# Performance work log

Measured on AMD Instinct MI355X. Metric: run time of the kernel, lower is better.

The kernel has to match this reference:

```python
import jax, jax.numpy as jnp
import numpy as np

B, H, W, C, WS, NCLS = 8, 256, 256, 256, 8, 18


def setup_inputs() -> dict:
    key = jax.random.key(0)
    ks = jax.random.split(key, 10)
    s = 1.0 / np.sqrt(C)
    return {
        "x": jax.random.normal(ks[0], (B, H, W, C), jnp.float32),
        "Wq": jax.random.normal(ks[1], (C, NCLS), jnp.float32) * s,
        "bq": jnp.zeros((NCLS,), jnp.float32),
        "Wk": jax.random.normal(ks[2], (C, NCLS), jnp.float32) * s,
        "bk": jnp.zeros((NCLS,), jnp.float32),
        "Wv": jax.random.normal(ks[3], (C, C), jnp.float32) * s,
        "bv": jnp.zeros((C,), jnp.float32),
        "Wres": jax.random.normal(ks[4], (C, C), jnp.float32) * s,
        "bres": jnp.zeros((C,), jnp.float32),
        "gamma": jnp.zeros((1,), jnp.float32) + 0.1,
    }


def _window_partition(x):
    # (B,H,W,C) -> (B*nH*nW, ws*ws, C)
    b, h, w, c = x.shape
    x = x.reshape(b, h // WS, WS, w // WS, WS, c)
    x = jnp.transpose(x, (0, 1, 3, 2, 4, 5))
    return x.reshape(-1, WS * WS, c)


def _window_reverse(xw, c):
    # (B*nH*nW, ws*ws, c) -> (B,H,W,c)
    x = xw.reshape(B, H // WS, W // WS, WS, WS, c)
    x = jnp.transpose(x, (0, 1, 3, 2, 4, 5))
    return x.reshape(B, H, W, c)


def reference(x, Wq, bq, Wk, bk, Wv, bv, Wres, bres, gamma):
    xw = _window_partition(x)                      # (nWin, ws^2, C)
    seg_map = xw @ Wq + bq                         # (nWin, ws^2, n_cls)
    seg_ft = xw @ Wk + bk                          # (nWin, ws^2, n_cls)
    feats = xw @ Wv + bv                           # (nWin, ws^2, C)
    score = jnp.einsum('nik,njk->nij', seg_map, seg_ft)  # (nWin, ws^2, ws^2)
    score = jax.nn.softmax(score, axis=-1)
    feats = jnp.einsum('nij,njc->nic', score, feats)
    feats = feats @ Wres + bres                    # dropout = identity (eval)
    feat_map = gamma * feats + xw
    return _window_reverse(seg_map, NCLS), _window_reverse(feat_map, C)
```

## Files before the change

kernel.cpp:

```cpp
#include <hip/hip_runtime.h>
#include <hip/hip_bf16.h>


typedef __bf16 bf16_t;
typedef __bf16 bf16x8 __attribute__((ext_vector_type(8)));
typedef __bf16 bf16x4 __attribute__((ext_vector_type(4)));
typedef float  f32x4  __attribute__((ext_vector_type(4)));

#define MFMA16(a, b, c) __builtin_amdgcn_mfma_f32_16x16x32_bf16((a), (b), (c), 0, 0, 0)
#define BAR() do { asm volatile("s_waitcnt lgkmcnt(0)" ::: "memory"); \
                   __builtin_amdgcn_s_barrier(); } while (0)

static constexpr int kC = 256, kNCLS = 18;
static constexpr int WQT_OFF = 0;
static constexpr int WKT_OFF = 8192;
static constexpr int WFT_OFF = 16384;
static constexpr int BF_BYTE_OFF = 81920 * 2;

__device__ __forceinline__ int xs_i(int r, int c) { return (r << 8) + (c ^ ((r & 7) << 3)); }
__device__ __forceinline__ int sb_i(int r, int c) { return (r << 6) + (c ^ ((r & 7) << 3)); }

__global__ __launch_bounds__(256) void prep_kernel(
    const float* __restrict__ Wq, const float* __restrict__ Wk,
    const float* __restrict__ Wv, const float* __restrict__ bv,
    const float* __restrict__ Wres, const float* __restrict__ bres,
    bf16_t* __restrict__ wsb, float* __restrict__ bff)
{
  const int blk = blockIdx.x, t = threadIdx.x;
  if (blk < 256) {
    __shared__ float wcol[256];
    const int n = blk;
    wcol[t] = Wres[t * kC + n];
    __syncthreads();
    float acc = 0.f;
    const float* wvrow = Wv + (size_t)t * kC;
#pragma unroll 4
    for (int j = 0; j < 256; j += 4) {
      f32x4 a = *(const f32x4*)(wvrow + j);
      acc += a[0] * wcol[j] + a[1] * wcol[j + 1] + a[2] * wcol[j + 2] + a[3] * wcol[j + 3];
    }
    wsb[WFT_OFF + n * kC + t] = (bf16_t)acc;
  } else if (blk == 256) {
    float acc = bres[t];
    for (int j = 0; j < 256; ++j) acc += bv[j] * Wres[j * kC + t];
    bff[t] = acc;
  } else {
    int tid = (blk - 257) * 256 + t;
    if (tid < 8192) {
      int n = tid >> 8, k = tid & 255;
      wsb[WQT_OFF + tid] = (n < kNCLS) ? (bf16_t)Wq[k * kNCLS + n] : (bf16_t)0.0f;
    } else {
      int u = tid - 8192;
      int n = u >> 8, k = u & 255;
      wsb[WKT_OFF + u] = (n < kNCLS) ? (bf16_t)Wk[k * kNCLS + n] : (bf16_t)0.0f;
    }
  }
}

__global__ __launch_bounds__(256, 2) void semwin_main(
    const float* __restrict__ x,
    const float* __restrict__ bq, const float* __restrict__ bk,
    const float* __restrict__ gamma,
    const bf16_t* __restrict__ wsb, const float* __restrict__ bff,
    float* __restrict__ out0, float* __restrict__ out1)
{
  __shared__ bf16_t xsf0[64 * 256];
  __shared__ bf16_t xsf1[64 * 256];
  __shared__ bf16_t sbf0[64 * 64];
  __shared__ bf16_t sbf1[64 * 64];

  const int tid  = threadIdx.x;
  const int wave = tid >> 6;
  const int lane = tid & 63;
  const int l15  = lane & 15;
  const int g    = lane >> 4;

  const int wid2 = blockIdx.x << 1;
  const int b    = wid2 >> 10;
  const int wh   = (wid2 >> 5) & 31;
  const int ww   = wid2 & 31;
  const int pix0 = (b << 16) + (wh << 11) + (ww << 3);
  const int pix1 = pix0 + 8;

  const f32x4 fzero = {0.f, 0.f, 0.f, 0.f};
  const float gm = gamma[0];

  {
    const int t = tid >> 2;
    const int q = tid & 3;
    const int ro = ((t >> 3) << 8) + (t & 7);
    const float* s0 = x + (size_t)(pix0 + ro) * kC + q * 8;
    const float* s1 = s0 + 8 * kC;
    f32x4 la[8][2], lb[8][2];
#pragma unroll
    for (int i = 0; i < 8; ++i) {
      la[i][0] = *(const f32x4*)(s0 + i * 32);
      la[i][1] = *(const f32x4*)(s0 + i * 32 + 4);
      lb[i][0] = *(const f32x4*)(s1 + i * 32);
      lb[i][1] = *(const f32x4*)(s1 + i * 32 + 4);
    }
#pragma unroll
    for (int i = 0; i < 8; ++i) {
      bf16x8 v0, v1;
#pragma unroll
      for (int r = 0; r < 4; ++r) {
        v0[r] = (bf16_t)la[i][0][r]; v0[4 + r] = (bf16_t)la[i][1][r];
        v1[r] = (bf16_t)lb[i][0][r]; v1[4 + r] = (bf16_t)lb[i][1][r];
      }
      *(bf16x8*)&xsf0[xs_i(t, i * 32 + q * 8)] = v0;
      *(bf16x8*)&xsf1[xs_i(t, i * 32 + q * 8)] = v1;
    }
  }
  BAR();

  {
    const bf16_t* wt   = wsb + ((wave < 2) ? WQT_OFF : WKT_OFF);
    const float*  bias = (wave < 2) ? bq : bk;
    const int mbase = (wave & 1) << 5;
    const int cofs  = (wave < 2) ? 0 : 32;
    const bool isQ  = (wave < 2);
    f32x4 acc[2][2][2];
#pragma unroll
    for (int w2 = 0; w2 < 2; ++w2)
#pragma unroll
      for (int mt = 0; mt < 2; ++mt)
#pragma unroll
        for (int nt = 0; nt < 2; ++nt) acc[w2][mt][nt] = fzero;
#pragma unroll
    for (int k0 = 0; k0 < 256; k0 += 32) {
      bf16x8 b0 = *(const bf16x8*)(wt + l15 * 256 + k0 + g * 8);
      bf16x8 b1 = *(const bf16x8*)(wt + (16 + l15) * 256 + k0 + g * 8);
#pragma unroll
      for (int w2 = 0; w2 < 2; ++w2) {
        const bf16_t* xs = w2 ? xsf1 : xsf0;
        bf16x8 a0 = *(const bf16x8*)&xs[xs_i(mbase + l15, k0 + g * 8)];
        bf16x8 a1 = *(const bf16x8*)&xs[xs_i(mbase + 16 + l15, k0 + g * 8)];
        acc[w2][0][0] = MFMA16(a0, b0, acc[w2][0][0]);
        acc[w2][0][1] = MFMA16(a0, b1, acc[w2][0][1]);
        acc[w2][1][0] = MFMA16(a1, b0, acc[w2][1][0]);
        acc[w2][1][1] = MFMA16(a1, b1, acc[w2][1][1]);
      }
    }
#pragma unroll
    for (int w2 = 0; w2 < 2; ++w2) {
      bf16_t* sb = w2 ? sbf1 : sbf0;
      const int pix = w2 ? pix1 : pix0;
#pragma unroll
      for (int nt = 0; nt < 2; ++nt) {
        const int coln = (nt << 4) + l15;
        const float bval = (coln < kNCLS) ? bias[coln] : 0.f;
#pragma unroll
        for (int mt = 0; mt < 2; ++mt) {
#pragma unroll
          for (int r = 0; r < 4; ++r) {
            const int row = mbase + (mt << 4) + (g << 2) + r;
            const float v = acc[w2][mt][nt][r] + bval;
            sb[sb_i(row, cofs + coln)] = (bf16_t)v;
            if (isQ && coln < kNCLS) {
              out0[(size_t)(pix + ((row >> 3) << 8) + (row & 7)) * kNCLS + coln] = v;
            }
          }
        }
      }
    }
  }
  BAR();

  {
    const int mbase = wave << 4;
    f32x4 s[2][4];
#pragma unroll
    for (int w2 = 0; w2 < 2; ++w2) {
      const bf16_t* sb = w2 ? sbf1 : sbf0;
      const bf16x8 aq = *(const bf16x8*)&sb[sb_i(mbase + l15, g * 8)];
#pragma unroll
      for (int nt = 0; nt < 4; ++nt) {
        bf16x8 bk8 = *(const bf16x8*)&sb[sb_i((nt << 4) + l15, 32 + g * 8)];
        s[w2][nt] = MFMA16(aq, bk8, fzero);
      }
    }
    BAR();
#pragma unroll
    for (int w2 = 0; w2 < 2; ++w2) {
      bf16_t* sb = w2 ? sbf1 : sbf0;
#pragma unroll
      for (int r = 0; r < 4; ++r) {
        float m = fmaxf(fmaxf(s[w2][0][r], s[w2][1][r]), fmaxf(s[w2][2][r], s[w2][3][r]));
#pragma unroll
        for (int off = 1; off < 16; off <<= 1) m = fmaxf(m, __shfl_xor(m, off));
        float e0 = __expf(s[w2][0][r] - m), e1 = __expf(s[w2][1][r] - m);
        float e2 = __expf(s[w2][2][r] - m), e3 = __expf(s[w2][3][r] - m);
        float sum = (e0 + e1) + (e2 + e3);
#pragma unroll
        for (int off = 1; off < 16; off <<= 1) sum += __shfl_xor(sum, off);
        const float inv = 1.0f / sum;
        const int row = mbase + (g << 2) + r;
        sb[sb_i(row, l15)]      = (bf16_t)(e0 * inv);
        sb[sb_i(row, 16 + l15)] = (bf16_t)(e1 * inv);
        sb[sb_i(row, 32 + l15)] = (bf16_t)(e2 * inv);
        sb[sb_i(row, 48 + l15)] = (bf16_t)(e3 * inv);
      }
    }
  }
  BAR();

  bf16x8 bp[2][4][2];
#pragma unroll
  for (int w2 = 0; w2 < 2; ++w2) {
    const bf16_t* sb = w2 ? sbf1 : sbf0;
#pragma unroll
    for (int nt = 0; nt < 4; ++nt) {
      bp[w2][nt][0] = *(const bf16x8*)&sb[sb_i((nt << 4) + l15, g * 8)];
      bp[w2][nt][1] = *(const bf16x8*)&sb[sb_i((nt << 4) + l15, 32 + g * 8)];
    }
  }

  auto bc_kloop = [&](int chunk, f32x4 (&accV)[2][4]) {
    const bf16_t* wft = wsb + WFT_OFF + (size_t)((chunk << 6) + (wave << 4)) * 256;
#pragma unroll
    for (int w2 = 0; w2 < 2; ++w2)
#pragma unroll
      for (int mt = 0; mt < 4; ++mt) accV[w2][mt] = fzero;
#pragma unroll
    for (int k0 = 0; k0 < 256; k0 += 32) {
      bf16x8 bf = *(const bf16x8*)(wft + l15 * 256 + k0 + g * 8);
#pragma unroll
      for (int w2 = 0; w2 < 2; ++w2) {
        const bf16_t* xs = w2 ? xsf1 : xsf0;
#pragma unroll
        for (int mt = 0; mt < 4; ++mt) {
          bf16x8 af = *(const bf16x8*)&xs[xs_i((mt << 4) + l15, k0 + g * 8)];
          accV[w2][mt] = MFMA16(af, bf, accV[w2][mt]);
        }
      }
    }
  };

  f32x4 accV[2][4];
  bc_kloop(0, accV);
  BAR();

  for (int chunk = 0; chunk < 4; ++chunk) {
    const int c2 = (chunk << 6) + (wave << 4) + (g << 2);
    const f32x4 bfv = *(const f32x4*)(bff + c2);
#pragma unroll
    for (int w2 = 0; w2 < 2; ++w2) {
      bf16_t* sb = w2 ? sbf1 : sbf0;
      const bf16_t* xs = w2 ? xsf1 : xsf0;
      const int pix = w2 ? pix1 : pix0;
#pragma unroll
      for (int mt = 0; mt < 4; ++mt) {
        bf16x4 pk;
#pragma unroll
        for (int r = 0; r < 4; ++r) pk[r] = (bf16_t)accV[w2][mt][r];
        *(bf16x4*)&sb[sb_i((wave << 4) + l15, (mt << 4) + (g << 2))] = pk;
      }
      const bf16x8 av0 = *(const bf16x8*)&sb[sb_i((wave << 4) + l15, g * 8)];
      const bf16x8 av1 = *(const bf16x8*)&sb[sb_i((wave << 4) + l15, 32 + g * 8)];
#pragma unroll
      for (int nt = 0; nt < 4; ++nt) {
        f32x4 accC = MFMA16(av0, bp[w2][nt][0], fzero);
        accC = MFMA16(av1, bp[w2][nt][1], accC);
        const int t = (nt << 4) + l15;
        const bf16x4 xv = *(const bf16x4*)&xs[xs_i(t, c2)];
        f32x4 o;
#pragma unroll
        for (int r = 0; r < 4; ++r)
          o[r] = gm * (accC[r] + bfv[r]) + (float)xv[r];
        *(f32x4*)(out1 + (size_t)(pix + ((t >> 3) << 8) + (t & 7)) * kC + c2) = o;
      }
    }
    if (chunk < 3) {
      bc_kloop(chunk + 1, accV);
      BAR();
    }
  }
}

extern "C" void kernel_launch(void* const* d_in, const int* in_sizes, int n_in,
                              void* d_out, int out_size, void* d_ws, size_t ws_size,
                              hipStream_t stream)
{
  const float* x     = (const float*)d_in[0];
  const float* Wq    = (const float*)d_in[1];
  const float* bq    = (const float*)d_in[2];
  const float* Wk    = (const float*)d_in[3];
  const float* bk    = (const float*)d_in[4];
  const float* Wv    = (const float*)d_in[5];
  const float* bv    = (const float*)d_in[6];
  const float* Wres  = (const float*)d_in[7];
  const float* bres  = (const float*)d_in[8];
  const float* gamma = (const float*)d_in[9];
  bf16_t* wsb = (bf16_t*)d_ws;
  float*  bff = (float*)((char*)d_ws + BF_BYTE_OFF);
  float* out0 = (float*)d_out;
  float* out1 = out0 + (size_t)8 * 256 * 256 * 18;

  prep_kernel<<<dim3(321), dim3(256), 0, stream>>>(Wq, Wk, Wv, bv, Wres, bres, wsb, bff);
  semwin_main<<<dim3(4096), dim3(256), 0, stream>>>(x, bq, bk, gamma, wsb, bff, out0, out1);
}
```

Baseline: 298.8 us.

## Hoist window A-fragments into registers and process windows sequentially per chunk

Restructures the feature GEMM stage so each of the two windows is handled in turn. All 32 A-operand fragments for the window are loaded from LDS into registers once and reused across the four output-channel chunks, so the same LDS data is no longer re-read for every chunk. This cuts LDS read traffic, but it holds many more live VGPRs and removes the previous overlap, where the next chunk's GEMM ran before the barrier. It also adds barriers, since the loop now runs over the windows serially.

```diff
diff --git a/kernel.cpp b/kernel.cpp
--- a/kernel.cpp
+++ b/kernel.cpp
@@ -204,63 +204,54 @@
   }
   BAR();
 
-  bf16x8 bp[2][4][2];
 #pragma unroll
   for (int w2 = 0; w2 < 2; ++w2) {
-    const bf16_t* sb = w2 ? sbf1 : sbf0;
+    const bf16_t* xs = w2 ? xsf1 : xsf0;
+    bf16_t* sb = w2 ? sbf1 : sbf0;
+    const int pix = w2 ? pix1 : pix0;
+
+    bf16x8 bp[4][2];
 #pragma unroll
     for (int nt = 0; nt < 4; ++nt) {
-      bp[w2][nt][0] = *(const bf16x8*)&sb[sb_i((nt << 4) + l15, g * 8)];
-      bp[w2][nt][1] = *(const bf16x8*)&sb[sb_i((nt << 4) + l15, 32 + g * 8)];
-    }
-  }
-
-  auto bc_kloop = [&](int chunk, f32x4 (&accV)[2][4]) {
-    const bf16_t* wft = wsb + WFT_OFF + (size_t)((chunk << 6) + (wave << 4)) * 256;
-#pragma unroll
-    for (int w2 = 0; w2 < 2; ++w2)
-#pragma unroll
-      for (int mt = 0; mt < 4; ++mt) accV[w2][mt] = fzero;
-#pragma unroll
-    for (int k0 = 0; k0 < 256; k0 += 32) {
-      bf16x8 bf = *(const bf16x8*)(wft + l15 * 256 + k0 + g * 8);
-#pragma unroll
-      for (int w2 = 0; w2 < 2; ++w2) {
-        const bf16_t* xs = w2 ? xsf1 : xsf0;
-#pragma unroll
-        for (int mt = 0; mt < 4; ++mt) {
-          bf16x8 af = *(const bf16x8*)&xs[xs_i((mt << 4) + l15, k0 + g * 8)];
-          accV[w2][mt] = MFMA16(af, bf, accV[w2][mt]);
-        }
-      }
-    }
-  };
-
-  f32x4 accV[2][4];
-  bc_kloop(0, accV);
-  BAR();
-
-  for (int chunk = 0; chunk < 4; ++chunk) {
-    const int c2 = (chunk << 6) + (wave << 4) + (g << 2);
-    const f32x4 bfv = *(const f32x4*)(bff + c2);
-#pragma unroll
-    for (int w2 = 0; w2 < 2; ++w2) {
-      bf16_t* sb = w2 ? sbf1 : sbf0;
-      const bf16_t* xs = w2 ? xsf1 : xsf0;
-      const int pix = w2 ? pix1 : pix0;
+      bp[nt][0] = *(const bf16x8*)&sb[sb_i((nt << 4) + l15, g * 8)];
+      bp[nt][1] = *(const bf16x8*)&sb[sb_i((nt << 4) + l15, 32 + g * 8)];
+    }
+    bf16x8 af[4][8];
+#pragma unroll
+    for (int mt = 0; mt < 4; ++mt)
+#pragma unroll
+      for (int kk = 0; kk < 8; ++kk)
+        af[mt][kk] = *(const bf16x8*)&xs[xs_i((mt << 4) + l15, kk * 32 + g * 8)];
+    BAR();
+
+    for (int chunk = 0; chunk < 4; ++chunk) {
+      const bf16_t* wft = wsb + WFT_OFF + (size_t)((chunk << 6) + (wave << 4)) * 256;
+      f32x4 accV[4];
+#pragma unroll
+      for (int mt = 0; mt < 4; ++mt) accV[mt] = fzero;
+#pragma unroll
+      for (int kk = 0; kk < 8; ++kk) {
+        bf16x8 bf = *(const bf16x8*)(wft + l15 * 256 + kk * 32 + g * 8);
+        accV[0] = MFMA16(af[0][kk], bf, accV[0]);
+        accV[1] = MFMA16(af[1][kk], bf, accV[1]);
+        accV[2] = MFMA16(af[2][kk], bf, accV[2]);
+        accV[3] = MFMA16(af[3][kk], bf, accV[3]);
+      }
 #pragma unroll
       for (int mt = 0; mt < 4; ++mt) {
         bf16x4 pk;
 #pragma unroll
-        for (int r = 0; r < 4; ++r) pk[r] = (bf16_t)accV[w2][mt][r];
+        for (int r = 0; r < 4; ++r) pk[r] = (bf16_t)accV[mt][r];
         *(bf16x4*)&sb[sb_i((wave << 4) + l15, (mt << 4) + (g << 2))] = pk;
       }
       const bf16x8 av0 = *(const bf16x8*)&sb[sb_i((wave << 4) + l15, g * 8)];
       const bf16x8 av1 = *(const bf16x8*)&sb[sb_i((wave << 4) + l15, 32 + g * 8)];
+      const int c2 = (chunk << 6) + (wave << 4) + (g << 2);
+      const f32x4 bfv = *(const f32x4*)(bff + c2);
 #pragma unroll
       for (int nt = 0; nt < 4; ++nt) {
-        f32x4 accC = MFMA16(av0, bp[w2][nt][0], fzero);
-        accC = MFMA16(av1, bp[w2][nt][1], accC);
+        f32x4 accC = MFMA16(av0, bp[nt][0], fzero);
+        accC = MFMA16(av1, bp[nt][1], accC);
         const int t = (nt << 4) + l15;
         const bf16x4 xv = *(const bf16x4*)&xs[xs_i(t, c2)];
         f32x4 o;
@@ -269,10 +260,7 @@
           o[r] = gm * (accC[r] + bfv[r]) + (float)xv[r];
         *(f32x4*)(out1 + (size_t)(pix + ((t >> 3) << 8) + (t & 7)) * kC + c2) = o;
       }
-    }
-    if (chunk < 3) {
-      bc_kloop(chunk + 1, accV);
-      BAR();
+      if (!(w2 == 1 && chunk == 3)) BAR();
     }
   }
 }
```

Measured after the change: 338.3 us. 1.13x slower.
